# Kernel optimization log

Hardware: AMD Instinct MI355X
Metric: run time of the kernel (lower is better)

Reference implementation:

```python
import jax, jax.numpy as jnp
import numpy as np

B, T, H = 128, 1024, 200
IN0, OUT = 8, 4  # GRU layer-0 input size (4 targets + 4 emotion), fc output dim


def setup_inputs() -> dict:
    key = jax.random.key(0)
    ks = jax.random.split(key, 12)
    s = 1.0 / np.sqrt(H)  # torch RNN default init: U(-1/sqrt(H), 1/sqrt(H))
    u = lambda k, shp: jax.random.uniform(k, shp, jnp.float32, -s, s)
    return {
        "x": jax.random.normal(ks[0], (B, T, IN0), jnp.float32),
        "W_ih0": u(ks[1], (3 * H, IN0)),
        "W_hh0": u(ks[2], (3 * H, H)),
        "b_ih0": u(ks[3], (3 * H,)),
        "b_hh0": u(ks[4], (3 * H,)),
        "W_ih1": u(ks[5], (3 * H, H)),
        "W_hh1": u(ks[6], (3 * H, H)),
        "b_ih1": u(ks[7], (3 * H,)),
        "b_hh1": u(ks[8], (3 * H,)),
        "W_fc": u(ks[9], (OUT, H)),
        "b_fc": u(ks[10], (OUT,)),
        "xlens": jax.random.randint(ks[11], (B,), 1, T + 1),
    }


def _gru_cell(h, gx, W_hh, b_hh):
    # torch GRU cell: gx = W_ih @ x + b_ih precomputed, gates order [r, z, n]
    gh = h @ W_hh.T + b_hh
    ir, iz, i_n = jnp.split(gx, 3, axis=-1)
    hr, hz, hn = jnp.split(gh, 3, axis=-1)
    r = jax.nn.sigmoid(ir + hr)
    z = jax.nn.sigmoid(iz + hz)
    n = jnp.tanh(i_n + r * hn)
    return (1.0 - z) * n + z * h


def _forward(x, W_ih0, W_hh0, b_ih0, b_hh0, W_ih1, W_hh1, b_ih1, b_hh1, W_fc, b_fc):
    b, t, _ = x.shape
    emotion = x[:, 0, -4:]                      # (B,4) frozen at t=0, as in source
    targets = x[:, :, :4]                       # (B,T,4)
    # step inputs: t=0 -> ones(B,4); t>0 -> targets[:, t-1] (teacher forcing)
    tf = jnp.concatenate([jnp.ones((b, 1, 4), x.dtype), targets[:, :-1, :]], axis=1)
    inputs = jnp.concatenate(
        [tf, jnp.broadcast_to(emotion[:, None, :], (b, t, 4))], axis=-1)  # (B,T,8)
    # precompute layer-0 input projections for all steps (one big GEMM)
    gx0 = jnp.einsum("btc,gc->btg", inputs, W_ih0) + b_ih0  # (B,T,3H)

    def step(carry, gx0_t):
        h0, h1 = carry
        h0 = _gru_cell(h0, gx0_t, W_hh0, b_hh0)
        gx1 = h0 @ W_ih1.T + b_ih1
        h1 = _gru_cell(h1, gx1, W_hh1, b_hh1)
        out = jnp.tanh(h1 @ W_fc.T + b_fc)      # fused fc + tanh
        return (h0, h1), out

    h0 = jnp.zeros((b, H), x.dtype)
    h1 = jnp.zeros((b, H), x.dtype)
    _, outs = jax.lax.scan(step, (h0, h1), jnp.swapaxes(gx0, 0, 1))  # (T,B,4)
    return jnp.swapaxes(outs, 0, 1)             # (B,T,4)


def reference(x, W_ih0, W_hh0, b_ih0, b_hh0, W_ih1, W_hh1, b_ih1, b_hh1, W_fc, b_fc, xlens):
    # xlens is accepted but unused, exactly as in the source forward()
    return _forward(x, W_ih0, W_hh0, b_ih0, b_hh0, W_ih1, W_hh1, b_ih1, b_hh1, W_fc, b_fc)
```

## Files before the change

kernel.cpp:

```cpp
#include <hip/hip_runtime.h>
#include <hip/hip_bf16.h>


#define TT 1024
#define HH 200
#define NB 16
#define HS 13
#define KP 232

typedef __attribute__((ext_vector_type(8))) short short8;
typedef __attribute__((ext_vector_type(4))) float f32x4;

__device__ __forceinline__ float sigm(float v) { return 1.0f / (1.0f + __expf(-v)); }
__device__ __forceinline__ float tanh_fast(float v) {
  float e = __expf(-2.0f * v);
  return (1.0f - e) / (1.0f + e);
}
__device__ __forceinline__ uint llc_load_u32(const uint* p) {
  return __hip_atomic_load(p, __ATOMIC_RELAXED, __HIP_MEMORY_SCOPE_SYSTEM);
}
__device__ __forceinline__ void llc_store_u32(uint* p, uint v) {
  __hip_atomic_store(p, v, __ATOMIC_RELAXED, __HIP_MEMORY_SCOPE_SYSTEM);
}
__device__ __forceinline__ float bfu2f(ushort u) {
  return __uint_as_float(((uint)u) << 16);
}
__device__ __forceinline__ ushort f2bfu(float f) {
  __hip_bfloat16 b = __float2bfloat16(f);
  return *(ushort*)&b;
}
__device__ __forceinline__ uint packf(float h) {
  ushort hi = f2bfu(h);
  float  fh = bfu2f(hi);
  ushort lo = f2bfu(h - fh);
  return (uint)hi | ((uint)lo << 16);
}

__global__ __launch_bounds__(256, 1) void gru2_mfma(
    const float* __restrict__ x,
    const float* __restrict__ Wih0, const float* __restrict__ Whh0,
    const float* __restrict__ bih0, const float* __restrict__ bhh0,
    const float* __restrict__ Wih1, const float* __restrict__ Whh1,
    const float* __restrict__ bih1, const float* __restrict__ bhh1,
    const float* __restrict__ Wfc,  const float* __restrict__ bfc,
    float* __restrict__ out,
    uint* __restrict__ h0g, uint* __restrict__ h1g, int* __restrict__ bars)
{
  __shared__ __align__(16) ushort hBh[2][NB][KP];
  __shared__ __align__(16) ushort hBl[2][NB][KP];
  __shared__ float D[117][17];
  __shared__ float Wi0[39][8];
  __shared__ float bi0[39], bh0[39], bi1[39], bh1[39], bfs[4];
  __shared__ float xc[NB][8];

  const int tid  = threadIdx.x;
  const int wave = tid >> 6;
  const int lane = tid & 63;
  const int m15  = lane & 15;
  const int q    = lane >> 4;

  const int g  = blockIdx.x & 7;
  const int s  = blockIdx.x >> 3;
  const int b0 = g * NB;
  const int j0 = s * HS;
  const int hs = (HH - j0 < HS) ? (HH - j0) : HS;
  const int th   = 3 * hs;
  const int h0r  = 6 * hs;
  const int T0   = (h0r + 15) >> 4;
  const int NT   = T0 + ((th + 15) >> 4);
  const bool isOut = (s == 15);

  short8 Ah[2][7], Al[2][7];
  #pragma unroll
  for (int mt = 0; mt < 2; ++mt) {
    const int T = wave * 2 + mt;
    const bool fc  = isOut && (wave == 2) && (mt == 0);
    const bool val = fc || (T < NT);
    #pragma unroll
    for (int kt = 0; kt < 7; ++kt) {
      short8 vh = {0,0,0,0,0,0,0,0}, vl = {0,0,0,0,0,0,0,0};
      #pragma unroll
      for (int j = 0; j < 8; ++j) {
        const int k = kt * 32 + q * 8 + j;
        float w = 0.0f;
        if (val && k < HH) {
          if (fc) {
            if (m15 < 4) w = Wfc[m15 * HH + k];
          } else {
            const int p = T * 16 + m15;
            int r = -1;
            if (p < h0r) r = p;
            else if (p >= T0 * 16 && (p - T0 * 16) < th) r = h0r + (p - T0 * 16);
            if (r >= 0) {
              const int m  = r / th, rr = r - m * th;
              const int qq = rr / hs, jj = rr - qq * hs;
              const float* src = (m == 0) ? Whh0 : ((m == 1) ? Wih1 : Whh1);
              w = src[(qq * HH + j0 + jj) * HH + k];
            }
          }
        }
        const ushort uh = f2bfu(w);
        const ushort ul = f2bfu(w - bfu2f(uh));
        vh[j] = (short)uh; vl[j] = (short)ul;
      }
      Ah[mt][kt] = vh; Al[mt][kt] = vl;
    }
  }

  for (int u = tid; u < th * 8; u += 256) {
    int rr = u >> 3, c = u & 7;
    int qq = rr / hs, jj = rr - qq * hs;
    Wi0[rr][c] = Wih0[(qq * HH + j0 + jj) * 8 + c];
  }
  for (int u = tid; u < th; u += 256) {
    int qq = u / hs, jj = u - qq * hs;
    int grow = qq * HH + j0 + jj;
    bi0[u] = bih0[grow]; bh0[u] = bhh0[grow];
    bi1[u] = bih1[grow]; bh1[u] = bhh1[grow];
  }
  if (tid < 4) bfs[tid] = bfc[tid];
  for (int u = tid; u < 2 * NB * KP / 2; u += 256) ((uint*)hBh)[u] = 0;
  for (int u = tid; u < 2 * NB * KP / 2; u += 256) ((uint*)hBl)[u] = 0;
  __syncthreads();

  int* bar = &bars[g * 64];
  const int cj = tid >> 4, cb = tid & 15;

  for (int t = 0; t <= TT + 1; ++t) {
    const uint* h0src = h0g + ((t + 1) & 1) * (128 * HH);
    const uint* h1src = h1g + (t & 1) * (128 * HH);
    uint tmp[25];
    #pragma unroll
    for (int i = 0; i < 25; ++i) {
      const int u  = tid + i * 256;
      const int st = u / 3200, rem = u - st * 3200;
      const int b  = rem / 200, k = rem - b * 200;
      tmp[i] = llc_load_u32(&(st ? h1src : h0src)[(b0 + b) * HH + k]);
    }
    #pragma unroll
    for (int i = 0; i < 25; ++i) {
      const int u  = tid + i * 256;
      const int st = u / 3200, rem = u - st * 3200;
      const int b  = rem / 200, k = rem - b * 200;
      hBh[st][b][k] = (ushort)(tmp[i] & 0xffff);
      hBl[st][b][k] = (ushort)(tmp[i] >> 16);
    }
    if (tid < 128 && t < TT) {
      int b = tid >> 3, c = tid & 7;
      float v;
      if (c < 4) v = (t == 0) ? 1.0f : x[((b0 + b) * TT + (t - 1)) * 8 + c];
      else       v = x[(b0 + b) * TT * 8 + c];
      xc[b][c] = v;
    }
    __syncthreads();

    #pragma unroll
    for (int mt = 0; mt < 2; ++mt) {
      const int T = wave * 2 + mt;
      const bool fc  = isOut && (wave == 2) && (mt == 0);
      const bool val = fc || (T < NT);
      if (!val) continue;
      const int st = fc ? 1 : ((T < T0) ? 0 : 1);
      const ushort* Bh = &hBh[st][m15][0];
      const ushort* Bl = &hBl[st][m15][0];
      f32x4 acc = {0.f, 0.f, 0.f, 0.f};
      #pragma unroll
      for (int kt = 0; kt < 7; ++kt) {
        const short8 bh = *(const short8*)&Bh[kt * 32 + q * 8];
        const short8 bl = *(const short8*)&Bl[kt * 32 + q * 8];
        acc = __builtin_amdgcn_mfma_f32_16x16x32_bf16(Ah[mt][kt], bh, acc, 0, 0, 0);
        acc = __builtin_amdgcn_mfma_f32_16x16x32_bf16(Ah[mt][kt], bl, acc, 0, 0, 0);
        acc = __builtin_amdgcn_mfma_f32_16x16x32_bf16(Al[mt][kt], bh, acc, 0, 0, 0);
      }
      if (fc) {
        if (t >= 2) {
          #pragma unroll
          for (int i = 0; i < 4; ++i) {
            const int p = q * 4 + i;
            if (p < 4)
              out[((b0 + m15) * TT + (t - 2)) * 4 + p] = tanh_fast(acc[i] + bfs[p]);
          }
        }
      } else {
        #pragma unroll
        for (int i = 0; i < 4; ++i) {
          const int p = T * 16 + q * 4 + i;
          int r = -1;
          if (p < h0r) r = p;
          else if (p >= T0 * 16 && (p - T0 * 16) < th) r = h0r + (p - T0 * 16);
          if (r >= 0) D[r][m15] = acc[i];
        }
      }
    }
    __syncthreads();

    if (cj < hs) {
      const float hv0 = bfu2f(hBh[0][cb][j0 + cj]) + bfu2f(hBl[0][cb][j0 + cj]);
      const float hv1 = bfu2f(hBh[1][cb][j0 + cj]) + bfu2f(hBl[1][cb][j0 + cj]);
      if (t < TT) {
        float ir = bi0[cj], iz = bi0[hs + cj], in_ = bi0[2 * hs + cj];
        #pragma unroll
        for (int c = 0; c < 8; ++c) {
          const float xv = xc[cb][c];
          ir  += Wi0[cj][c] * xv;
          iz  += Wi0[hs + cj][c] * xv;
          in_ += Wi0[2 * hs + cj][c] * xv;
        }
        const float hr = D[cj][cb] + bh0[cj];
        const float hz = D[hs + cj][cb] + bh0[hs + cj];
        const float hn = D[2 * hs + cj][cb] + bh0[2 * hs + cj];
        const float r = sigm(ir + hr), z = sigm(iz + hz);
        const float n = tanh_fast(in_ + r * hn);
        llc_store_u32(&h0g[(t & 1) * (128 * HH) + (b0 + cb) * HH + j0 + cj],
                      packf((1.0f - z) * n + z * hv0));
      }
      if (t >= 1 && t <= TT) {
        const float ir  = D[3 * hs + cj][cb] + bi1[cj];
        const float iz  = D[4 * hs + cj][cb] + bi1[hs + cj];
        const float in_ = D[5 * hs + cj][cb] + bi1[2 * hs + cj];
        const float hr  = D[6 * hs + cj][cb] + bh1[cj];
        const float hz  = D[7 * hs + cj][cb] + bh1[hs + cj];
        const float hn  = D[8 * hs + cj][cb] + bh1[2 * hs + cj];
        const float r = sigm(ir + hr), z = sigm(iz + hz);
        const float n = tanh_fast(in_ + r * hn);
        llc_store_u32(&h1g[((t + 1) & 1) * (128 * HH) + (b0 + cb) * HH + j0 + cj],
                      packf((1.0f - z) * n + z * hv1));
      }
    }

    __syncthreads();
    if (tid == 0) {
      __hip_atomic_fetch_add(bar, 1, __ATOMIC_RELAXED, __HIP_MEMORY_SCOPE_SYSTEM);
      const int target = 16 * (t + 1);
      while (__hip_atomic_load(bar, __ATOMIC_RELAXED, __HIP_MEMORY_SCOPE_SYSTEM) < target)
        __builtin_amdgcn_s_sleep(1);
    }
    __syncthreads();
  }
}

extern "C" void kernel_launch(void* const* d_in, const int* in_sizes, int n_in,
                              void* d_out, int out_size, void* d_ws, size_t ws_size,
                              hipStream_t stream) {
  uint* ws = (uint*)d_ws;
  hipMemsetAsync(d_ws, 0, (size_t)(102400 + 512) * sizeof(uint), stream);
  gru2_mfma<<<128, 256, 0, stream>>>(
      (const float*)d_in[0],
      (const float*)d_in[1], (const float*)d_in[2],
      (const float*)d_in[3], (const float*)d_in[4],
      (const float*)d_in[5], (const float*)d_in[6],
      (const float*)d_in[7], (const float*)d_in[8],
      (const float*)d_in[9], (const float*)d_in[10],
      (float*)d_out, ws, ws + 51200, (int*)(ws + 102400));
}
```

Measured before the change: 3.170 ms.

## Replace atomic barrier with parity-tagged hidden state and halve batch per block

Drops the per-group atomic counter barrier. Each block now spins on the hidden-state words themselves, which carry a parity tag in the LSB of the low bf16 part. The batch per block drops from 16 to 8, so the grid grows to 256 blocks at two blocks per CU. The x input projection for the r and z gates is folded into the MFMA through extra K columns, and the hi/lo halves are stored as packed uint and split with perm. The fc output is computed by a different tile. The tag costs one bit of low-part precision, and the direct spin-polling has a correctness risk around memory ordering.

```diff
diff --git a/kernel.cpp b/kernel.cpp
--- a/kernel.cpp
+++ b/kernel.cpp
@@ -2,11 +2,12 @@
 #include <hip/hip_bf16.h>
 
 
-#define TT 1024
-#define HH 200
-#define NB 16
-#define HS 13
-#define KP 232
+#define TT   1024
+#define HH   200
+#define NBB  8
+#define HS   13
+#define KP   228
+#define HBUF 25600
 
 typedef __attribute__((ext_vector_type(8))) short short8;
 typedef __attribute__((ext_vector_type(4))) float f32x4;
@@ -22,21 +23,31 @@
 __device__ __forceinline__ void llc_store_u32(uint* p, uint v) {
   __hip_atomic_store(p, v, __ATOMIC_RELAXED, __HIP_MEMORY_SCOPE_SYSTEM);
 }
-__device__ __forceinline__ float bfu2f(ushort u) {
-  return __uint_as_float(((uint)u) << 16);
-}
+__device__ __forceinline__ float bfu2f(ushort u) { return __uint_as_float(((uint)u) << 16); }
 __device__ __forceinline__ ushort f2bfu(float f) {
   __hip_bfloat16 b = __float2bfloat16(f);
   return *(ushort*)&b;
 }
-__device__ __forceinline__ uint packf(float h) {
+__device__ __forceinline__ uint packf_tag(float h, uint tag) {
   ushort hi = f2bfu(h);
-  float  fh = bfu2f(hi);
-  ushort lo = f2bfu(h - fh);
-  return (uint)hi | ((uint)lo << 16);
-}
-
-__global__ __launch_bounds__(256, 1) void gru2_mfma(
+  ushort lo = f2bfu(h - bfu2f(hi));
+  return (uint)hi | ((((uint)lo & 0xFFFEu) | tag) << 16);
+}
+__device__ __forceinline__ uint packf_nt(float h) {
+  ushort hi = f2bfu(h);
+  ushort lo = f2bfu(h - bfu2f(hi));
+  return (uint)hi | (((uint)lo) << 16);
+}
+__device__ __forceinline__ float upk(uint u) {
+  return __uint_as_float(u << 16) + __uint_as_float(u & 0xFFFF0000u);
+}
+
+__global__ void init_state(uint* p) {
+  int i = blockIdx.x * 256 + threadIdx.x;
+  if (i < 4 * HBUF) llc_store_u32(p + i, 0x00010000u);
+}
+
+__global__ __launch_bounds__(256, 2) void gru2_tag(
     const float* __restrict__ x,
     const float* __restrict__ Wih0, const float* __restrict__ Whh0,
     const float* __restrict__ bih0, const float* __restrict__ bhh0,
@@ -44,14 +55,14 @@
     const float* __restrict__ bih1, const float* __restrict__ bhh1,
     const float* __restrict__ Wfc,  const float* __restrict__ bfc,
     float* __restrict__ out,
-    uint* __restrict__ h0g, uint* __restrict__ h1g, int* __restrict__ bars)
+    uint* __restrict__ h0g, uint* __restrict__ h1g)
 {
-  __shared__ __align__(16) ushort hBh[2][NB][KP];
-  __shared__ __align__(16) ushort hBl[2][NB][KP];
-  __shared__ float D[117][17];
-  __shared__ float Wi0[39][8];
-  __shared__ float bi0[39], bh0[39], bi1[39], bh1[39], bfs[4];
-  __shared__ float xc[NB][8];
+  __shared__ __align__(16) uint hB[2][NBB][KP];
+  __shared__ float D[128][9];
+  __shared__ float xc[2][NBB][8];
+  __shared__ float Wi0n[HS][8];
+  __shared__ float bs0rz[2 * HS], b0ni[HS], b0nh[HS];
+  __shared__ float bs1rz[2 * HS], b1ni[HS], b1nh[HS], bfcs[4];
 
   const int tid  = threadIdx.x;
   const int wave = tid >> 6;
@@ -59,183 +70,230 @@
   const int m15  = lane & 15;
   const int q    = lane >> 4;
 
-  const int g  = blockIdx.x & 7;
-  const int s  = blockIdx.x >> 3;
-  const int b0 = g * NB;
+  const int g  = blockIdx.x & 15;
+  const int s  = blockIdx.x >> 4;
+  const int b0 = g * NBB;
   const int j0 = s * HS;
   const int hs = (HH - j0 < HS) ? (HH - j0) : HS;
-  const int th   = 3 * hs;
-  const int h0r  = 6 * hs;
-  const int T0   = (h0r + 15) >> 4;
-  const int NT   = T0 + ((th + 15) >> 4);
+  const int th  = 3 * hs;
+  const int h0r = 6 * hs;
+  const int T0  = (h0r + 15) >> 4;
+  const int NT  = T0 + ((th + 15) >> 4);
   const bool isOut = (s == 15);
 
   short8 Ah[2][7], Al[2][7];
   #pragma unroll
-  for (int mt = 0; mt < 2; ++mt) {
-    const int T = wave * 2 + mt;
-    const bool fc  = isOut && (wave == 2) && (mt == 0);
-    const bool val = fc || (T < NT);
+  for (int tt = 0; tt < 2; ++tt) {
+    const int T = 2 * wave + tt;
+    const bool isFC = isOut && (T == NT);
+    const bool val  = (T < NT) || isFC;
     #pragma unroll
     for (int kt = 0; kt < 7; ++kt) {
       short8 vh = {0,0,0,0,0,0,0,0}, vl = {0,0,0,0,0,0,0,0};
-      #pragma unroll
-      for (int j = 0; j < 8; ++j) {
-        const int k = kt * 32 + q * 8 + j;
-        float w = 0.0f;
-        if (val && k < HH) {
-          if (fc) {
-            if (m15 < 4) w = Wfc[m15 * HH + k];
+      if (val) {
+        #pragma unroll
+        for (int j = 0; j < 8; ++j) {
+          const int k = kt * 32 + q * 8 + j;
+          float w = 0.0f;
+          const int p = T * 16 + m15;
+          if (isFC) {
+            if (m15 < 4 && k < HH) w = Wfc[m15 * HH + k];
           } else {
-            const int p = T * 16 + m15;
             int r = -1;
             if (p < h0r) r = p;
-            else if (p >= T0 * 16 && (p - T0 * 16) < th) r = h0r + (p - T0 * 16);
+            else { int pp = p - T0 * 16; if (pp >= 0 && pp < th) r = h0r + pp; }
             if (r >= 0) {
-              const int m  = r / th, rr = r - m * th;
-              const int qq = rr / hs, jj = rr - qq * hs;
-              const float* src = (m == 0) ? Whh0 : ((m == 1) ? Wih1 : Whh1);
-              w = src[(qq * HH + j0 + jj) * HH + k];
+              const int m = r / th, rr = r - m * th;
+              const int q3 = rr / hs, jj = rr - q3 * hs;
+              const int grow = q3 * HH + j0 + jj;
+              if (k < HH) {
+                const float* src = (m == 0) ? Whh0 : ((m == 1) ? Wih1 : Whh1);
+                w = src[grow * HH + k];
+              } else if (k < 208 && m == 0 && q3 < 2) {
+                w = Wih0[grow * 8 + (k - HH)];
+              }
             }
           }
-        }
-        const ushort uh = f2bfu(w);
-        const ushort ul = f2bfu(w - bfu2f(uh));
-        vh[j] = (short)uh; vl[j] = (short)ul;
-      }
-      Ah[mt][kt] = vh; Al[mt][kt] = vl;
-    }
-  }
-
-  for (int u = tid; u < th * 8; u += 256) {
-    int rr = u >> 3, c = u & 7;
-    int qq = rr / hs, jj = rr - qq * hs;
-    Wi0[rr][c] = Wih0[(qq * HH + j0 + jj) * 8 + c];
-  }
-  for (int u = tid; u < th; u += 256) {
-    int qq = u / hs, jj = u - qq * hs;
-    int grow = qq * HH + j0 + jj;
-    bi0[u] = bih0[grow]; bh0[u] = bhh0[grow];
-    bi1[u] = bih1[grow]; bh1[u] = bhh1[grow];
-  }
-  if (tid < 4) bfs[tid] = bfc[tid];
-  for (int u = tid; u < 2 * NB * KP / 2; u += 256) ((uint*)hBh)[u] = 0;
-  for (int u = tid; u < 2 * NB * KP / 2; u += 256) ((uint*)hBl)[u] = 0;
+          const ushort hi = f2bfu(w);
+          const ushort lo = f2bfu(w - bfu2f(hi));
+          vh[j] = (short)hi; vl[j] = (short)lo;
+        }
+      }
+      Ah[tt][kt] = vh; Al[tt][kt] = vl;
+    }
+  }
+
+  for (int u = tid; u < 2 * NBB * KP; u += 256) (&hB[0][0][0])[u] = 0;
+  for (int u = tid; u < 2 * hs; u += 256) {
+    const int q3 = u / hs, jj = u - q3 * hs;
+    const int grow = q3 * HH + j0 + jj;
+    bs0rz[u] = bih0[grow] + bhh0[grow];
+    bs1rz[u] = bih1[grow] + bhh1[grow];
+  }
+  for (int u = tid; u < hs; u += 256) {
+    const int grow = 2 * HH + j0 + u;
+    b0ni[u] = bih0[grow]; b0nh[u] = bhh0[grow];
+    b1ni[u] = bih1[grow]; b1nh[u] = bhh1[grow];
+  }
+  for (int u = tid; u < hs * 8; u += 256) {
+    const int jj = u >> 3, c = u & 7;
+    Wi0n[jj][c] = Wih0[(2 * HH + j0 + jj) * 8 + c];
+  }
+  if (tid < 4) bfcs[tid] = bfc[tid];
+
+  int boff[13], lofs[13]; uint stm = 0;
+  #pragma unroll
+  for (int i = 0; i < 13; ++i) {
+    const int u = tid + i * 256;
+    if (u < 3200) {
+      const int st = (u >= 1600) ? 1 : 0;
+      const int rem = u - st * 1600;
+      const int b = rem / 200, k = rem - b * 200;
+      boff[i] = (b0 + b) * HH + k;
+      lofs[i] = (st * NBB + b) * KP + k;
+      if (st) stm |= (1u << i);
+    } else { boff[i] = 0; lofs[i] = 0; }
+  }
+  uint* const hBf = &hB[0][0][0];
+
+  const int cj = tid & 15;
+  const int cb = tid >> 4;
+  const bool gateAct = (cj < hs) && (cb < 8);
+
   __syncthreads();
 
-  int* bar = &bars[g * 64];
-  const int cj = tid >> 4, cb = tid & 15;
-
   for (int t = 0; t <= TT + 1; ++t) {
-    const uint* h0src = h0g + ((t + 1) & 1) * (128 * HH);
-    const uint* h1src = h1g + (t & 1) * (128 * HH);
-    uint tmp[25];
+    const uint e0 = (uint)(((t - 1) >> 1) & 1);
+    const uint e1 = (uint)(((t - 2) >> 1) & 1);
+    const uint* h0s = h0g + ((t + 1) & 1) * HBUF;
+    const uint* h1s = h1g + (t & 1) * HBUF;
+    const bool chk0 = (t <= TT);
+    uint v[13];
     #pragma unroll
-    for (int i = 0; i < 25; ++i) {
-      const int u  = tid + i * 256;
-      const int st = u / 3200, rem = u - st * 3200;
-      const int b  = rem / 200, k = rem - b * 200;
-      tmp[i] = llc_load_u32(&(st ? h1src : h0src)[(b0 + b) * HH + k]);
+    for (int i = 0; i < 13; ++i)
+      if (i < 12 || tid < 128)
+        v[i] = llc_load_u32((((stm >> i) & 1) ? h1s : h0s) + boff[i]);
+    for (;;) {
+      bool ok = true;
+      #pragma unroll
+      for (int i = 0; i < 13; ++i)
+        if (i < 12 || tid < 128) {
+          const bool st = (stm >> i) & 1;
+          if (st || chk0) ok = ok && (((v[i] >> 16) & 1u) == (st ? e1 : e0));
+        }
+      if (ok) break;
+      #pragma unroll
+      for (int i = 0; i < 13; ++i)
+        if (i < 12 || tid < 128)
+          v[i] = llc_load_u32((((stm >> i) & 1) ? h1s : h0s) + boff[i]);
     }
     #pragma unroll
-    for (int i = 0; i < 25; ++i) {
-      const int u  = tid + i * 256;
-      const int st = u / 3200, rem = u - st * 3200;
-      const int b  = rem / 200, k = rem - b * 200;
-      hBh[st][b][k] = (ushort)(tmp[i] & 0xffff);
-      hBl[st][b][k] = (ushort)(tmp[i] >> 16);
-    }
-    if (tid < 128 && t < TT) {
-      int b = tid >> 3, c = tid & 7;
-      float v;
-      if (c < 4) v = (t == 0) ? 1.0f : x[((b0 + b) * TT + (t - 1)) * 8 + c];
-      else       v = x[(b0 + b) * TT * 8 + c];
-      xc[b][c] = v;
+    for (int i = 0; i < 13; ++i)
+      if (i < 12 || tid < 128) hBf[lofs[i]] = v[i];
+
+    if (tid < 64 && t < TT) {
+      const int b = tid >> 3, c = tid & 7;
+      float xv;
+      if (c < 4) xv = (t == 0) ? 1.0f : x[((b0 + b) * TT + (t - 1)) * 8 + c];
+      else       xv = x[(b0 + b) * TT * 8 + c];
+      xc[t & 1][b][c] = xv;
+      hB[0][b][HH + c] = packf_nt(xv);
     }
     __syncthreads();
 
-    #pragma unroll
-    for (int mt = 0; mt < 2; ++mt) {
-      const int T = wave * 2 + mt;
-      const bool fc  = isOut && (wave == 2) && (mt == 0);
-      const bool val = fc || (T < NT);
-      if (!val) continue;
-      const int st = fc ? 1 : ((T < T0) ? 0 : 1);
-      const ushort* Bh = &hBh[st][m15][0];
-      const ushort* Bl = &hBl[st][m15][0];
-      f32x4 acc = {0.f, 0.f, 0.f, 0.f};
+    float hv0 = 0.f, hv1 = 0.f;
+    if (gateAct) {
+      hv0 = upk(hB[0][cb][j0 + cj]);
+      hv1 = upk(hB[1][cb][j0 + cj]);
+    }
+
+    {
+      const int Ta = 2 * wave, Tb = Ta + 1;
+      const bool fa = isOut && (Ta == NT), fb = isOut && (Tb == NT);
+      const bool va = (Ta < NT) || fa, vb = (Tb < NT) || fb;
+      const int sa = (Ta < T0) ? 0 : 1, sb = (Tb < T0) ? 0 : 1;
+      f32x4 acc0 = {0.f,0.f,0.f,0.f}, acc1 = {0.f,0.f,0.f,0.f};
+      const uint* rowp = &hB[0][m15 & 7][0];
       #pragma unroll
-      for (int kt = 0; kt < 7; ++kt) {
-        const short8 bh = *(const short8*)&Bh[kt * 32 + q * 8];
-        const short8 bl = *(const short8*)&Bl[kt * 32 + q * 8];
-        acc = __builtin_amdgcn_mfma_f32_16x16x32_bf16(Ah[mt][kt], bh, acc, 0, 0, 0);
-        acc = __builtin_amdgcn_mfma_f32_16x16x32_bf16(Ah[mt][kt], bl, acc, 0, 0, 0);
-        acc = __builtin_amdgcn_mfma_f32_16x16x32_bf16(Al[mt][kt], bh, acc, 0, 0, 0);
-      }
-      if (fc) {
-        if (t >= 2) {
+      for (int st = 0; st < 2; ++st) {
+        const bool nA = va && (sa == st), nB = vb && (sb == st);
+        if (!(nA || nB)) continue;
+        const uint* rp = rowp + st * (NBB * KP);
+        short8 Bh[7], Bl[7];
+        #pragma unroll
+        for (int kt = 0; kt < 7; ++kt) {
+          const uint4 u0 = *(const uint4*)&rp[kt * 32 + q * 8];
+          const uint4 u1 = *(const uint4*)&rp[kt * 32 + q * 8 + 4];
+          union { uint u[4]; short8 s; } ch, cl;
+          ch.u[0] = __builtin_amdgcn_perm(u0.y, u0.x, 0x05040100u);
+          ch.u[1] = __builtin_amdgcn_perm(u0.w, u0.z, 0x05040100u);
+          ch.u[2] = __builtin_amdgcn_perm(u1.y, u1.x, 0x05040100u);
+          ch.u[3] = __builtin_amdgcn_perm(u1.w, u1.z, 0x05040100u);
+          cl.u[0] = __builtin_amdgcn_perm(u0.y, u0.x, 0x07060302u);
+          cl.u[1] = __builtin_amdgcn_perm(u0.w, u0.z, 0x07060302u);
+          cl.u[2] = __builtin_amdgcn_perm(u1.y, u1.x, 0x07060302u);
+          cl.u[3] = __builtin_amdgcn_perm(u1.w, u1.z, 0x07060302u);
+          Bh[kt] = ch.s; Bl[kt] = cl.s;
+        }
+        if (nA) {
           #pragma unroll
-          for (int i = 0; i < 4; ++i) {
-            const int p = q * 4 + i;
-            if (p < 4)
-              out[((b0 + m15) * TT + (t - 2)) * 4 + p] = tanh_fast(acc[i] + bfs[p]);
+          for (int kt = 0; kt < 7; ++kt) {
+            acc0 = __builtin_amdgcn_mfma_f32_16x16x32_bf16(Ah[0][kt], Bh[kt], acc0, 0, 0, 0);
+            acc0 = __builtin_amdgcn_mfma_f32_16x16x32_bf16(Ah[0][kt], Bl[kt], acc0, 0, 0, 0);
+            acc0 = __builtin_amdgcn_mfma_f32_16x16x32_bf16(Al[0][kt], Bh[kt], acc0, 0, 0, 0);
           }
         }
-      } else {
+        if (nB) {
+          #pragma unroll
+          for (int kt = 0; kt < 7; ++kt) {
+            acc1 = __builtin_amdgcn_mfma_f32_16x16x32_bf16(Ah[1][kt], Bh[kt], acc1, 0, 0, 0);
+            acc1 = __builtin_amdgcn_mfma_f32_16x16x32_bf16(Ah[1][kt], Bl[kt], acc1, 0, 0, 0);
+            acc1 = __builtin_amdgcn_mfma_f32_16x16x32_bf16(Al[1][kt], Bh[kt], acc1, 0, 0, 0);
+          }
+        }
+      }
+      if (m15 < 8) {
+        if (va) {
+          #pragma unroll
+          for (int i = 0; i < 4; ++i) D[Ta * 16 + q * 4 + i][m15] = acc0[i];
+        }
+        if (vb) {
+          #pragma unroll
+          for (int i = 0; i < 4; ++i) D[Tb * 16 + q * 4 + i][m15] = acc1[i];
+        }
+      }
+    }
+    __syncthreads();
+
+    if (gateAct) {
+      if (t < TT) {
+        const float sr = D[cj][cb] + bs0rz[cj];
+        const float sz = D[hs + cj][cb] + bs0rz[hs + cj];
+        const float hn = D[2 * hs + cj][cb] + b0nh[cj];
+        float in0 = b0ni[cj];
         #pragma unroll
-        for (int i = 0; i < 4; ++i) {
-          const int p = T * 16 + q * 4 + i;
-          int r = -1;
-          if (p < h0r) r = p;
-          else if (p >= T0 * 16 && (p - T0 * 16) < th) r = h0r + (p - T0 * 16);
-          if (r >= 0) D[r][m15] = acc[i];
-        }
-      }
-    }
-    __syncthreads();
-
-    if (cj < hs) {
-      const float hv0 = bfu2f(hBh[0][cb][j0 + cj]) + bfu2f(hBl[0][cb][j0 + cj]);
-      const float hv1 = bfu2f(hBh[1][cb][j0 + cj]) + bfu2f(hBl[1][cb][j0 + cj]);
-      if (t < TT) {
-        float ir = bi0[cj], iz = bi0[hs + cj], in_ = bi0[2 * hs + cj];
-        #pragma unroll
-        for (int c = 0; c < 8; ++c) {
-          const float xv = xc[cb][c];
-          ir  += Wi0[cj][c] * xv;
-          iz  += Wi0[hs + cj][c] * xv;
-          in_ += Wi0[2 * hs + cj][c] * xv;
-        }
-        const float hr = D[cj][cb] + bh0[cj];
-        const float hz = D[hs + cj][cb] + bh0[hs + cj];
-        const float hn = D[2 * hs + cj][cb] + bh0[2 * hs + cj];
-        const float r = sigm(ir + hr), z = sigm(iz + hz);
-        const float n = tanh_fast(in_ + r * hn);
-        llc_store_u32(&h0g[(t & 1) * (128 * HH) + (b0 + cb) * HH + j0 + cj],
-                      packf((1.0f - z) * n + z * hv0));
+        for (int c = 0; c < 8; ++c) in0 += Wi0n[cj][c] * xc[t & 1][cb][c];
+        const float r = sigm(sr), z = sigm(sz);
+        const float n = tanh_fast(in0 + r * hn);
+        llc_store_u32(h0g + (t & 1) * HBUF + (b0 + cb) * HH + (j0 + cj),
+                      packf_tag((1.0f - z) * n + z * hv0, (uint)((t >> 1) & 1)));
       }
       if (t >= 1 && t <= TT) {
-        const float ir  = D[3 * hs + cj][cb] + bi1[cj];
-        const float iz  = D[4 * hs + cj][cb] + bi1[hs + cj];
-        const float in_ = D[5 * hs + cj][cb] + bi1[2 * hs + cj];
-        const float hr  = D[6 * hs + cj][cb] + bh1[cj];
-        const float hz  = D[7 * hs + cj][cb] + bh1[hs + cj];
-        const float hn  = D[8 * hs + cj][cb] + bh1[2 * hs + cj];
-        const float r = sigm(ir + hr), z = sigm(iz + hz);
-        const float n = tanh_fast(in_ + r * hn);
-        llc_store_u32(&h1g[((t + 1) & 1) * (128 * HH) + (b0 + cb) * HH + j0 + cj],
-                      packf((1.0f - z) * n + z * hv1));
-      }
-    }
-
-    __syncthreads();
-    if (tid == 0) {
-      __hip_atomic_fetch_add(bar, 1, __ATOMIC_RELAXED, __HIP_MEMORY_SCOPE_SYSTEM);
-      const int target = 16 * (t + 1);
-      while (__hip_atomic_load(bar, __ATOMIC_RELAXED, __HIP_MEMORY_SCOPE_SYSTEM) < target)
-        __builtin_amdgcn_s_sleep(1);
-    }
-    __syncthreads();
+        const int pd = T0 * 16 + cj;
+        const float sr  = D[3 * hs + cj][cb] + D[pd][cb] + bs1rz[cj];
+        const float sz  = D[4 * hs + cj][cb] + D[pd + hs][cb] + bs1rz[hs + cj];
+        const float in1 = D[5 * hs + cj][cb] + b1ni[cj];
+        const float hn1 = D[pd + 2 * hs][cb] + b1nh[cj];
+        const float r = sigm(sr), z = sigm(sz);
+        const float n = tanh_fast(in1 + r * hn1);
+        llc_store_u32(h1g + ((t + 1) & 1) * HBUF + (b0 + cb) * HH + (j0 + cj),
+                      packf_tag((1.0f - z) * n + z * hv1, (uint)(((t - 1) >> 1) & 1)));
+      }
+    }
+    if (isOut && t >= 2 && tid < 32) {
+      const int oo = tid & 3, ob = tid >> 2;
+      out[((b0 + ob) * TT + (t - 2)) * 4 + oo] = tanh_fast(D[48 + oo][ob] + bfcs[oo]);
+    }
   }
 }
 
@@ -243,13 +301,13 @@
                               void* d_out, int out_size, void* d_ws, size_t ws_size,
                               hipStream_t stream) {
   uint* ws = (uint*)d_ws;
-  hipMemsetAsync(d_ws, 0, (size_t)(102400 + 512) * sizeof(uint), stream);
-  gru2_mfma<<<128, 256, 0, stream>>>(
+  init_state<<<400, 256, 0, stream>>>(ws);
+  gru2_tag<<<256, 256, 0, stream>>>(
       (const float*)d_in[0],
       (const float*)d_in[1], (const float*)d_in[2],
       (const float*)d_in[3], (const float*)d_in[4],
       (const float*)d_in[5], (const float*)d_in[6],
       (const float*)d_in[7], (const float*)d_in[8],
       (const float*)d_in[9], (const float*)d_in[10],
-      (float*)d_out, ws, ws + 51200, (int*)(ws + 102400));
-}
+      (float*)d_out, ws, ws + 2 * HBUF);
+}
```

Result: slower. 6.246 ms (+97.0%).
